# Kernel optimization log

Hardware: AMD Instinct MI355X
Metric: run time of the kernel (lower is better)

The kernel has to match this reference:

```python
import jax, jax.numpy as jnp
import numpy as np

N, E, IN_DIM, HID, HEADS = 50000, 800000, 128, 16, 8
EPS_BN = 1e-5


def _gat_conv(x, edge_index, W, att_src, att_dst, bias, heads, out_ch, concat):
    # x: [N, F_in]; W: [heads*out_ch, F_in]; att_*: [heads, out_ch]
    n = x.shape[0]
    h = (x @ W.T).reshape(n, heads, out_ch)            # [N, H, C]
    a_src = (h * att_src[None]).sum(-1)                # [N, H]
    a_dst = (h * att_dst[None]).sum(-1)                # [N, H]
    src, dst = edge_index[0], edge_index[1]
    alpha = jax.nn.leaky_relu(a_src[src] + a_dst[dst], negative_slope=0.2)  # [E, H]
    # segment softmax over destination node (per head)
    amax = jax.ops.segment_max(alpha, dst, num_segments=n)
    amax = jnp.where(jnp.isfinite(amax), amax, 0.0)
    ex = jnp.exp(alpha - amax[dst])
    denom = jax.ops.segment_sum(ex, dst, num_segments=n)
    attn = ex / (denom[dst] + 1e-16)                   # [E, H]
    msg = h[src] * attn[:, :, None]                    # [E, H, C]
    out = jax.ops.segment_sum(msg, dst, num_segments=n)  # [N, H, C]
    out = out.reshape(n, heads * out_ch) if concat else out.mean(axis=1)
    return out + bias


def _bn_eval(h, mean, var, gamma, beta):
    return (h - mean) * jax.lax.rsqrt(var + EPS_BN) * gamma + beta


def setup_inputs() -> dict:
    key = jax.random.key(0)
    ks = jax.random.split(key, 16)
    s = 0.1
    inp = {
        "x": jax.random.normal(ks[0], (N, IN_DIM), jnp.float32),
        "edge_index": jax.random.randint(ks[1], (2, E), 0, N, jnp.int32),
        # layer 0: GATConv(128 -> 16, heads=8, concat)
        "w0": jax.random.normal(ks[2], (HEADS * HID, IN_DIM), jnp.float32) * s,
        "asrc0": jax.random.normal(ks[3], (HEADS, HID), jnp.float32) * s,
        "adst0": jax.random.normal(ks[4], (HEADS, HID), jnp.float32) * s,
        "b0": jnp.zeros((HEADS * HID,), jnp.float32),
        "skip0": jax.random.normal(ks[5], (HEADS * HID, IN_DIM), jnp.float32) * s,
        "bn0_g": jnp.ones((HEADS * HID,), jnp.float32),
        "bn0_b": jnp.zeros((HEADS * HID,), jnp.float32),
        "bn0_m": jax.random.normal(ks[6], (HEADS * HID,), jnp.float32) * s,
        "bn0_v": jax.random.uniform(ks[7], (HEADS * HID,), jnp.float32, 0.5, 1.5),
        # layer 1: GATConv(128 -> 16, heads=1, concat=False)
        "w1": jax.random.normal(ks[8], (HID, HEADS * HID), jnp.float32) * s,
        "asrc1": jax.random.normal(ks[9], (1, HID), jnp.float32) * s,
        "adst1": jax.random.normal(ks[10], (1, HID), jnp.float32) * s,
        "b1": jnp.zeros((HID,), jnp.float32),
        "skip1": jax.random.normal(ks[11], (HID, HEADS * HID), jnp.float32) * s,
        "bn1_g": jnp.ones((HID,), jnp.float32),
        "bn1_b": jnp.zeros((HID,), jnp.float32),
        "bn1_m": jax.random.normal(ks[12], (HID,), jnp.float32) * s,
        "bn1_v": jax.random.uniform(ks[13], (HID,), jnp.float32, 0.5, 1.5),
    }
    return inp


def reference(x, edge_index, w0, asrc0, adst0, b0, skip0, bn0_g, bn0_b, bn0_m, bn0_v,
              w1, asrc1, adst1, b1, skip1, bn1_g, bn1_b, bn1_m, bn1_v):
    # eval mode: dropout = identity, BN uses running stats
    h_in = x
    h = _gat_conv(h_in, edge_index, w0, asrc0, adst0, b0, HEADS, HID, True)   # [N, 128]
    h = _bn_eval(h, bn0_m, bn0_v, bn0_g, bn0_b)
    h = h + h_in @ skip0.T
    h = jax.nn.elu(h)
    h_in = h
    h = _gat_conv(h_in, edge_index, w1, asrc1, adst1, b1, 1, HID, False)      # [N, 16]
    h = _bn_eval(h, bn1_m, bn1_v, bn1_g, bn1_b)
    h = h + h_in @ skip1.T
    h = jax.nn.elu(h)
    return h
```

## Files before the change

### kernel.cpp

```cpp
#include <hip/hip_runtime.h>
#include <hip/hip_bf16.h>

#define NN 50000
#define EE 800000
#define INDIM 128
#define HIDC 16
#define NHEAD 8
#define COARSE 196
#define EPB 2048
#define CAPR 6144
#define CAPB 8192

typedef __attribute__((ext_vector_type(8))) short bf16x8;
typedef __attribute__((ext_vector_type(4))) float f32x4;

__device__ __forceinline__ float bf2f(unsigned short u) {
    union { float f; unsigned int i; } v; v.i = ((unsigned int)u) << 16; return v.f;
}
__device__ __forceinline__ unsigned short f2bf(float f) {
    union { float f; unsigned int i; } v; v.f = f;
    unsigned int r = v.i + 0x7FFFu + ((v.i >> 16) & 1u);
    return (unsigned short)(r >> 16);
}
__device__ __forceinline__ unsigned char f2fp8(float f) {
    return (unsigned char)(__builtin_amdgcn_cvt_pk_fp8_f32(f, f, 0, 0) & 0xFF);
}

__global__ __launch_bounds__(256) void k_cvt(const float* __restrict__ x,
                                             const float* __restrict__ w0,
                                             const float* __restrict__ skip0,
                                             const float* __restrict__ w1,
                                             const float* __restrict__ skip1,
                                             unsigned int* __restrict__ xb2,
                                             unsigned int* __restrict__ wb2,
                                             unsigned int* __restrict__ wb1_2,
                                             int* __restrict__ ccur)
{
    if (blockIdx.x == 0 && threadIdx.x < COARSE)
        ccur[threadIdx.x] = threadIdx.x * CAPR;

    const long NX = (long)NN * 128 / 4;
    const long NW = 256 * 128 / 4;
    const long NW1 = 32 * 128 / 4;
    long i = (long)blockIdx.x * 256 + threadIdx.x;
    if (i < NX) {
        float4 v = ((const float4*)x)[i];
        xb2[i * 2]     = (unsigned int)f2bf(v.x) | ((unsigned int)f2bf(v.y) << 16);
        xb2[i * 2 + 1] = (unsigned int)f2bf(v.z) | ((unsigned int)f2bf(v.w) << 16);
    } else if (i < NX + NW) {
        long j = i - NX;
        const float4* src = (j < 128 * 128 / 4) ? ((const float4*)w0 + j)
                                                : ((const float4*)skip0 + (j - 128 * 128 / 4));
        float4 v = *src;
        wb2[j * 2]     = (unsigned int)f2bf(v.x) | ((unsigned int)f2bf(v.y) << 16);
        wb2[j * 2 + 1] = (unsigned int)f2bf(v.z) | ((unsigned int)f2bf(v.w) << 16);
    } else if (i < NX + NW + NW1) {
        long j = i - NX - NW;
        const float4* src = (j < 16 * 128 / 4) ? ((const float4*)w1 + j)
                                               : ((const float4*)skip1 + (j - 16 * 128 / 4));
        float4 v = *src;
        wb1_2[j * 2]     = (unsigned int)f2bf(v.x) | ((unsigned int)f2bf(v.y) << 16);
        wb1_2[j * 2 + 1] = (unsigned int)f2bf(v.z) | ((unsigned int)f2bf(v.w) << 16);
    }
}

__global__ __launch_bounds__(256) void k_partA(const int* __restrict__ ei,
                                               int* __restrict__ ccur,
                                               unsigned int* __restrict__ pairs)
{
    __shared__ int bcnt[256];
    __shared__ int lofs[256];
    __shared__ int gofs[256];
    __shared__ unsigned int stage[EPB];
    __shared__ int gpos[EPB];
    const int t = threadIdx.x;
    const int e0 = blockIdx.x * EPB;

    bcnt[t] = 0;
    __syncthreads();

    int mybin[8], myrank[8];
    unsigned int mypair[8];
    #pragma unroll
    for (int k = 0; k < 8; k++) {
        int e = e0 + k * 256 + t;
        mybin[k] = -1;
        if (e < EE) {
            int s = ei[e], d = ei[EE + e];
            int b = d >> 8;
            myrank[k] = atomicAdd(&bcnt[b], 1);
            mybin[k] = b;
            mypair[k] = ((unsigned)d << 16) | (unsigned)s;
        }
    }
    __syncthreads();

    int v = bcnt[t];
    lofs[t] = v;
    __syncthreads();
    for (int off = 1; off < 256; off <<= 1) {
        int u = (t >= off) ? lofs[t - off] : 0;
        __syncthreads();
        lofs[t] += u;
        __syncthreads();
    }
    if (t < COARSE && v > 0) gofs[t] = atomicAdd(&ccur[t], v);
    __syncthreads();

    #pragma unroll
    for (int k = 0; k < 8; k++) {
        int b = mybin[k];
        if (b >= 0) {
            int slot = (lofs[b] - bcnt[b]) + myrank[k];
            stage[slot] = mypair[k];
            gpos[slot]  = gofs[b] + myrank[k];
        }
    }
    __syncthreads();

    const int total = lofs[255];
    for (int i = t; i < total; i += 256)
        pairs[gpos[i]] = stage[i];
}

__global__ __launch_bounds__(256) void k_partB(const unsigned int* __restrict__ pairs,
                                               const int* __restrict__ ccur,
                                               unsigned short* __restrict__ srcidx,
                                               int* __restrict__ rowbeg,
                                               int* __restrict__ deg)
{
    __shared__ int fcnt[256], fofs[256], fcur[256];
    __shared__ unsigned short stage[CAPB];
    const int b = blockIdx.x, t = threadIdx.x;
    const int beg = b * CAPR;
    int cnt = ccur[b] - beg;
    if (cnt > CAPR) cnt = CAPR;

    fcnt[t] = 0;
    __syncthreads();
    for (int i = t; i < cnt; i += 256) {
        unsigned int d = pairs[beg + i] >> 16;
        atomicAdd(&fcnt[d & 255], 1);
    }
    __syncthreads();

    int v = fcnt[t];
    fofs[t] = v;
    __syncthreads();
    for (int off = 1; off < 256; off <<= 1) {
        int u = (t >= off) ? fofs[t - off] : 0;
        __syncthreads();
        fofs[t] += u;
        __syncthreads();
    }
    int ex = fofs[t] - v;
    int node = b * 256 + t;
    if (node < NN) { rowbeg[node] = beg + ex; deg[node] = v; }
    fcur[t] = ex;
    __syncthreads();

    for (int i = t; i < cnt; i += 256) {
        unsigned int p = pairs[beg + i];
        unsigned int d = p >> 16;
        int slot = atomicAdd(&fcur[d & 255], 1);
        stage[slot] = (unsigned short)(p & 0xFFFFu);
    }
    __syncthreads();
    for (int i = t; i < cnt; i += 256)
        srcidx[beg + i] = stage[i];
}

__global__ __launch_bounds__(256) void k_gemm0(
    const unsigned short* __restrict__ xb, const unsigned short* __restrict__ wb,
    const float* __restrict__ asrc0, const float* __restrict__ adst0,
    unsigned char* __restrict__ h0f, unsigned short* __restrict__ s0b,
    float* __restrict__ a_src0, float* __restrict__ a_dst0)
{
    const int wave = threadIdx.x >> 6;
    const int lane = threadIdx.x & 63;
    const int lrow = lane & 15;
    const int quad = lane >> 4;
    const int rowbase = blockIdx.x * 64;

    bf16x8 bfrag[4][4];
    float asv[4], adv[4];
    #pragma unroll
    for (int t = 0; t < 4; t++) {
        const int jg = wave * 64 + t * 16 + lrow;
        #pragma unroll
        for (int ki = 0; ki < 4; ki++)
            bfrag[t][ki] = *(const bf16x8*)(wb + (long)jg * 128 + ki * 32 + quad * 8);
        if (wave < 2) { asv[t] = asrc0[jg]; adv[t] = adst0[jg]; }
    }

    #pragma unroll
    for (int sub = 0; sub < 4; sub++) {
        const int row0 = rowbase + sub * 16;
        if (row0 >= NN) break;
        const unsigned short* xrow = xb + (long)(row0 + lrow) * 128;
        bf16x8 afrag[4];
        #pragma unroll
        for (int ki = 0; ki < 4; ki++)
            afrag[ki] = *(const bf16x8*)(xrow + ki * 32 + quad * 8);

        f32x4 acc[4];
        #pragma unroll
        for (int t = 0; t < 4; t++) acc[t] = (f32x4){0.f, 0.f, 0.f, 0.f};

        #pragma unroll
        for (int ki = 0; ki < 4; ki++)
            #pragma unroll
            for (int t = 0; t < 4; t++)
                acc[t] = __builtin_amdgcn_mfma_f32_16x16x32_bf16(afrag[ki], bfrag[t][ki], acc[t], 0, 0, 0);

        if (wave < 2) {
            #pragma unroll
            for (int t = 0; t < 4; t++) {
                const int jg = wave * 64 + t * 16 + lrow;
                #pragma unroll
                for (int r = 0; r < 4; r++) {
                    const int n = row0 + quad * 4 + r;
                    float val = acc[t][r];
                    h0f[(long)n * 128 + jg] = f2fp8(val);
                    float ps = val * asv[t];
                    float pd = val * adv[t];
                    ps += __shfl_xor(ps, 1); ps += __shfl_xor(ps, 2);
                    ps += __shfl_xor(ps, 4); ps += __shfl_xor(ps, 8);
                    pd += __shfl_xor(pd, 1); pd += __shfl_xor(pd, 2);
                    pd += __shfl_xor(pd, 4); pd += __shfl_xor(pd, 8);
                    if (lrow == 0) {
                        const int h = wave * 4 + t;
                        a_src0[(long)n * 8 + h] = ps;
                        a_dst0[(long)n * 8 + h] = pd;
                    }
                }
            }
        } else {
            #pragma unroll
            for (int t = 0; t < 4; t++) {
                const int jg = wave * 64 + t * 16 + lrow - 128;
                #pragma unroll
                for (int r = 0; r < 4; r++) {
                    const int n = row0 + quad * 4 + r;
                    s0b[(long)n * 128 + jg] = f2bf(acc[t][r]);
                }
            }
        }
    }
}

__global__ __launch_bounds__(256) void k_agg0(
    const int* __restrict__ rowbeg, const int* __restrict__ deg,
    const unsigned short* __restrict__ srcidx,
    const unsigned char* __restrict__ h0f, const float* __restrict__ a_src0,
    const float* __restrict__ a_dst0, unsigned int* __restrict__ out0b2)
{
    const int d = (blockIdx.x * 256 + threadIdx.x) >> 6;
    if (d >= NN) return;
    const int lane = threadIdx.x & 63;
    const int beg = rowbeg[d], end = beg + deg[d];
    const int eslot = lane >> 3;
    const int hph1 = lane & 7;
    const int c = lane * 2;
    const int hsel = lane >> 3;
    const float adst = a_dst0[(long)d * 8 + hph1];

    float den = 0.f;
    float2 accA = {0.f, 0.f}, accB = {0.f, 0.f};
    for (int i = beg; i < end; i += 16) {
        const int idxA = i + eslot;
        const int idxB = i + 8 + eslot;
        const bool vA = idxA < end;
        const bool vB = idxB < end;
        const int sA = vA ? (int)srcidx[idxA] : 0;
        const int sB = vB ? (int)srcidx[idxB] : 0;
        float aA = a_src0[(long)sA * 8 + hph1] + adst;
        float aB = a_src0[(long)sB * 8 + hph1] + adst;
        aA = aA > 0.f ? aA : 0.2f * aA;
        aB = aB > 0.f ? aB : 0.2f * aB;
        const float wA = vA ? __expf(aA) : 0.f;
        const float wB = vB ? __expf(aB) : 0.f;
        den += wA + wB;
        #pragma unroll
        for (int j = 0; j < 8; j++) {
            const float wjA = __shfl(wA, j * 8 + hsel);
            const int sjA = __shfl(sA, j * 8);
            const float wjB = __shfl(wB, j * 8 + hsel);
            const int sjB = __shfl(sB, j * 8);
            const unsigned int uA = *(const unsigned short*)(h0f + (long)sjA * 128 + c);
            const unsigned int uB = *(const unsigned short*)(h0f + (long)sjB * 128 + c);
            accA.x += wjA * __builtin_amdgcn_cvt_f32_fp8(uA, 0);
            accA.y += wjA * __builtin_amdgcn_cvt_f32_fp8(uA, 1);
            accB.x += wjB * __builtin_amdgcn_cvt_f32_fp8(uB, 0);
            accB.y += wjB * __builtin_amdgcn_cvt_f32_fp8(uB, 1);
        }
    }
    float2 acc = {accA.x + accB.x, accA.y + accB.y};
    den += __shfl_xor(den, 8);
    den += __shfl_xor(den, 16);
    den += __shfl_xor(den, 32);
    const float denh = __shfl(den, hsel);
    const float inv = 1.f / (denh + 1e-16f);
    out0b2[(long)d * 64 + lane] =
        (unsigned int)f2bf(acc.x * inv) | ((unsigned int)f2bf(acc.y * inv) << 16);
}

__global__ __launch_bounds__(256) void k_post0(
    const unsigned short* __restrict__ out0b, const unsigned short* __restrict__ s0b,
    const float* __restrict__ b0, const float* __restrict__ g0,
    const float* __restrict__ bb0, const float* __restrict__ m0,
    const float* __restrict__ v0,
    const unsigned short* __restrict__ wb1,
    const float* __restrict__ asrc1, const float* __restrict__ adst1,
    unsigned short* __restrict__ h1b, float* __restrict__ s1,
    float* __restrict__ a_src1, float* __restrict__ a_dst1)
{
    __shared__ float Ac[128], Bc[128];
    const int tid = threadIdx.x;
    if (tid < 128) {
        float A = g0[tid] * rsqrtf(v0[tid] + 1e-5f);
        Ac[tid] = A;
        Bc[tid] = (b0[tid] - m0[tid]) * A + bb0[tid];
    }
    __syncthreads();

    const int lane = tid & 63, wave = tid >> 6;
    const int lrow = lane & 15, quad = lane >> 4;

    bf16x8 bfrag[2][4];
    #pragma unroll
    for (int t = 0; t < 2; t++)
        #pragma unroll
        for (int ki = 0; ki < 4; ki++)
            bfrag[t][ki] = *(const bf16x8*)(wb1 + (long)(t * 16 + lrow) * 128 + ki * 32 + quad * 8);
    const float avec = asrc1[lrow];
    const float dvec = adst1[lrow];

    const int tile = blockIdx.x * 4 + wave;
    if (tile * 16 >= NN) return;
    const int n0 = tile * 16;
    const long arow = (long)(n0 + lrow) * 128;

    bf16x8 afrag[4];
    #pragma unroll
    for (int ki = 0; ki < 4; ki++) {
        const int ch = ki * 32 + quad * 8;
        uint4 uo = *(const uint4*)(out0b + arow + ch);
        uint4 us = *(const uint4*)(s0b + arow + ch);
        const unsigned int uov[4] = {uo.x, uo.y, uo.z, uo.w};
        const unsigned int usv[4] = {us.x, us.y, us.z, us.w};
        bf16x8 af;
        #pragma unroll
        for (int e = 0; e < 4; e++) {
            const int c0 = ch + e * 2, c1 = c0 + 1;
            float x0 = bf2f((unsigned short)uov[e]) * Ac[c0] + Bc[c0] + bf2f((unsigned short)usv[e]);
            float x1 = bf2f((unsigned short)(uov[e] >> 16)) * Ac[c1] + Bc[c1] + bf2f((unsigned short)(usv[e] >> 16));
            x0 = x0 > 0.f ? x0 : __expf(x0) - 1.f;
            x1 = x1 > 0.f ? x1 : __expf(x1) - 1.f;
            af[e * 2]     = (short)f2bf(x0);
            af[e * 2 + 1] = (short)f2bf(x1);
        }
        afrag[ki] = af;
    }

    f32x4 acc0 = (f32x4){0.f, 0.f, 0.f, 0.f};
    f32x4 acc1 = (f32x4){0.f, 0.f, 0.f, 0.f};
    #pragma unroll
    for (int ki = 0; ki < 4; ki++) {
        acc0 = __builtin_amdgcn_mfma_f32_16x16x32_bf16(afrag[ki], bfrag[0][ki], acc0, 0, 0, 0);
        acc1 = __builtin_amdgcn_mfma_f32_16x16x32_bf16(afrag[ki], bfrag[1][ki], acc1, 0, 0, 0);
    }

    #pragma unroll
    for (int r = 0; r < 4; r++) {
        const int node = n0 + quad * 4 + r;
        h1b[(long)node * 16 + lrow] = f2bf(acc0[r]);
        s1[(long)node * 16 + lrow] = acc1[r];
        float ps = acc0[r] * avec;
        float pd = acc0[r] * dvec;
        ps += __shfl_xor(ps, 1); ps += __shfl_xor(ps, 2);
        ps += __shfl_xor(ps, 4); ps += __shfl_xor(ps, 8);
        pd += __shfl_xor(pd, 1); pd += __shfl_xor(pd, 2);
        pd += __shfl_xor(pd, 4); pd += __shfl_xor(pd, 8);
        if (lrow == 0) { a_src1[node] = ps; a_dst1[node] = pd; }
    }
}

__global__ __launch_bounds__(256) void k_agg1_final(
    const int* __restrict__ rowbeg, const int* __restrict__ deg,
    const unsigned short* __restrict__ srcidx,
    const unsigned short* __restrict__ h1b, const float* __restrict__ a_src1,
    const float* __restrict__ a_dst1, const float* __restrict__ s1,
    const float* __restrict__ b1, const float* __restrict__ g1,
    const float* __restrict__ bb1, const float* __restrict__ m1,
    const float* __restrict__ v1, float* __restrict__ out)
{
    const int gid = blockIdx.x * 256 + threadIdx.x;
    const int d = gid >> 3;
    if (d >= NN) return;
    const int lane = threadIdx.x & 63;
    const int gl = lane & 7;
    const int gb = lane & ~7;
    const int c0 = gl * 2, c1 = c0 + 1;
    const int beg = rowbeg[d], end = beg + deg[d];
    const float adst = a_dst1[d];

    float den = 0.f;
    float2 accA = {0.f, 0.f}, accB = {0.f, 0.f};
    for (int i = beg; i < end; i += 16) {
        const int idxA = i + gl;
        const int idxB = i + 8 + gl;
        const bool vA = idxA < end;
        const bool vB = idxB < end;
        const int sA = vA ? (int)srcidx[idxA] : 0;
        const int sB = vB ? (int)srcidx[idxB] : 0;
        float aA = a_src1[sA] + adst;
        float aB = a_src1[sB] + adst;
        aA = aA > 0.f ? aA : 0.2f * aA;
        aB = aB > 0.f ? aB : 0.2f * aB;
        const float wA = vA ? __expf(aA) : 0.f;
        const float wB = vB ? __expf(aB) : 0.f;
        den += wA + wB;
        #pragma unroll
        for (int j = 0; j < 8; j++) {
            const float wjA = __shfl(wA, gb | j);
            const int sjA = __shfl(sA, gb | j);
            const float wjB = __shfl(wB, gb | j);
            const int sjB = __shfl(sB, gb | j);
            const unsigned int uA = *(const unsigned int*)(h1b + (long)sjA * 16 + c0);
            const unsigned int uB = *(const unsigned int*)(h1b + (long)sjB * 16 + c0);
            accA.x += wjA * bf2f((unsigned short)uA);
            accA.y += wjA * bf2f((unsigned short)(uA >> 16));
            accB.x += wjB * bf2f((unsigned short)uB);
            accB.y += wjB * bf2f((unsigned short)(uB >> 16));
        }
    }
    float2 acc = {accA.x + accB.x, accA.y + accB.y};
    den += __shfl_xor(den, 1);
    den += __shfl_xor(den, 2);
    den += __shfl_xor(den, 4);
    const float inv = 1.f / (den + 1e-16f);

    const float A0 = g1[c0] * rsqrtf(v1[c0] + 1e-5f);
    const float B0 = (b1[c0] - m1[c0]) * A0 + bb1[c0];
    const float A1 = g1[c1] * rsqrtf(v1[c1] + 1e-5f);
    const float B1 = (b1[c1] - m1[c1]) * A1 + bb1[c1];
    float2 sv = *(const float2*)(s1 + (long)d * 16 + c0);
    float v0o = acc.x * inv * A0 + B0 + sv.x;
    float v1o = acc.y * inv * A1 + B1 + sv.y;
    v0o = v0o > 0.f ? v0o : __expf(v0o) - 1.f;
    v1o = v1o > 0.f ? v1o : __expf(v1o) - 1.f;
    *(float2*)(out + (long)d * 16 + c0) = make_float2(v0o, v1o);
}

extern "C" void kernel_launch(void* const* d_in, const int* in_sizes, int n_in,
                              void* d_out, int out_size, void* d_ws, size_t ws_size,
                              hipStream_t stream)
{
    (void)in_sizes; (void)n_in; (void)out_size; (void)ws_size;
    const float* x     = (const float*)d_in[0];
    const int*   ei    = (const int*)d_in[1];
    const float* w0    = (const float*)d_in[2];
    const float* asrc0 = (const float*)d_in[3];
    const float* adst0 = (const float*)d_in[4];
    const float* b0    = (const float*)d_in[5];
    const float* skip0 = (const float*)d_in[6];
    const float* bn0g  = (const float*)d_in[7];
    const float* bn0b  = (const float*)d_in[8];
    const float* bn0m  = (const float*)d_in[9];
    const float* bn0v  = (const float*)d_in[10];
    const float* w1    = (const float*)d_in[11];
    const float* asrc1 = (const float*)d_in[12];
    const float* adst1 = (const float*)d_in[13];
    const float* b1    = (const float*)d_in[14];
    const float* skip1 = (const float*)d_in[15];
    const float* bn1g  = (const float*)d_in[16];
    const float* bn1b  = (const float*)d_in[17];
    const float* bn1m  = (const float*)d_in[18];
    const float* bn1v  = (const float*)d_in[19];

    const long NPAIR = (long)COARSE * CAPR;
    unsigned int* pairs = (unsigned int*)d_ws;
    unsigned short* xb    = (unsigned short*)(pairs + NPAIR);
    unsigned short* wb    = xb + (long)NN * 128;
    unsigned short* wb1   = wb + 256 * 128;
    unsigned short* s0b   = wb1 + 32 * 128;
    unsigned short* out0b = s0b + (long)NN * 128;
    unsigned short* h1b   = out0b + (long)NN * 128;
    unsigned short* srcidx= h1b + (long)NN * 16;
    unsigned char*  h0f   = (unsigned char*)(srcidx + NPAIR);
    float* a_src0 = (float*)(h0f + (long)NN * 128);
    float* a_dst0 = a_src0 + (long)NN * 8;
    float* s1     = a_dst0 + (long)NN * 8;
    float* a_src1 = s1 + (long)NN * 16;
    float* a_dst1 = a_src1 + NN;
    int* ccur   = (int*)(a_dst1 + NN);
    int* rowbeg = ccur + COARSE;
    int* deg    = rowbeg + NN;

    const long NTOT = (long)NN * 128 / 4 + 256 * 128 / 4 + 32 * 128 / 4;
    k_cvt<<<(unsigned)((NTOT + 255) / 256), 256, 0, stream>>>(
        x, w0, skip0, w1, skip1,
        (unsigned int*)xb, (unsigned int*)wb, (unsigned int*)wb1, ccur);

    k_partA<<<(EE + EPB - 1) / EPB, 256, 0, stream>>>(ei, ccur, pairs);
    k_partB<<<COARSE, 256, 0, stream>>>(pairs, ccur, srcidx, rowbeg, deg);

    k_gemm0<<<(NN + 63) / 64, 256, 0, stream>>>(xb, wb, asrc0, adst0,
                                                h0f, s0b, a_src0, a_dst0);
    k_agg0<<<(NN * 64 + 255) / 256, 256, 0, stream>>>(rowbeg, deg, srcidx, h0f,
                                                      a_src0, a_dst0, (unsigned int*)out0b);
    k_post0<<<(NN / 16 + 3) / 4, 256, 0, stream>>>(out0b, s0b, b0, bn0g, bn0b, bn0m, bn0v,
                                                   wb1, asrc1, adst1, h1b, s1, a_src1, a_dst1);
    k_agg1_final<<<(NN * 8 + 255) / 256, 256, 0, stream>>>(rowbeg, deg, srcidx, h1b,
                                                           a_src1, a_dst1, s1,
                                                           b1, bn1g, bn1b, bn1m, bn1v,
                                                           (float*)d_out);
}
```

Measured before the change: 218.2 us.

## Transpose MFMA operands in gemm0 for packed row-contiguous stores

Swaps the A and B operands of the MFMA in the first-layer GEMM so that each lane holds four consecutive output columns of a single node. The FP8 h0 values and BF16 skip values can then be written as packed 4-byte and 8-byte stores instead of scattered single-element stores, and the attention dot products are reduced with two cross-quad shuffles instead of four. It also halves rows per block (64 to 32) to launch twice as many blocks. The change targets store efficiency in the GEMM epilogue; the smaller tile reloads the weight fragments more often per row.

```diff
diff --git a/kernel.cpp b/kernel.cpp
--- a/kernel.cpp
+++ b/kernel.cpp
@@ -21,9 +21,6 @@
     union { float f; unsigned int i; } v; v.f = f;
     unsigned int r = v.i + 0x7FFFu + ((v.i >> 16) & 1u);
     return (unsigned short)(r >> 16);
-}
-__device__ __forceinline__ unsigned char f2fp8(float f) {
-    return (unsigned char)(__builtin_amdgcn_cvt_pk_fp8_f32(f, f, 0, 0) & 0xFF);
 }
 
 __global__ __launch_bounds__(256) void k_cvt(const float* __restrict__ x,
@@ -180,21 +177,25 @@
     const int lane = threadIdx.x & 63;
     const int lrow = lane & 15;
     const int quad = lane >> 4;
-    const int rowbase = blockIdx.x * 64;
+    const int rowbase = blockIdx.x * 32;
 
     bf16x8 bfrag[4][4];
-    float asv[4], adv[4];
+    float4 asv[4], adv[4];
     #pragma unroll
     for (int t = 0; t < 4; t++) {
         const int jg = wave * 64 + t * 16 + lrow;
         #pragma unroll
         for (int ki = 0; ki < 4; ki++)
             bfrag[t][ki] = *(const bf16x8*)(wb + (long)jg * 128 + ki * 32 + quad * 8);
-        if (wave < 2) { asv[t] = asrc0[jg]; adv[t] = adst0[jg]; }
-    }
-
-    #pragma unroll
-    for (int sub = 0; sub < 4; sub++) {
+        if (wave < 2) {
+            const int cb = wave * 64 + t * 16 + quad * 4;
+            asv[t] = *(const float4*)(asrc0 + cb);
+            adv[t] = *(const float4*)(adst0 + cb);
+        }
+    }
+
+    #pragma unroll
+    for (int sub = 0; sub < 2; sub++) {
         const int row0 = rowbase + sub * 16;
         if (row0 >= NN) break;
         const unsigned short* xrow = xb + (long)(row0 + lrow) * 128;
@@ -211,39 +212,36 @@
         for (int ki = 0; ki < 4; ki++)
             #pragma unroll
             for (int t = 0; t < 4; t++)
-                acc[t] = __builtin_amdgcn_mfma_f32_16x16x32_bf16(afrag[ki], bfrag[t][ki], acc[t], 0, 0, 0);
-
+                acc[t] = __builtin_amdgcn_mfma_f32_16x16x32_bf16(bfrag[t][ki], afrag[ki], acc[t], 0, 0, 0);
+
+        const int node = row0 + lrow;
         if (wave < 2) {
             #pragma unroll
             for (int t = 0; t < 4; t++) {
-                const int jg = wave * 64 + t * 16 + lrow;
-                #pragma unroll
-                for (int r = 0; r < 4; r++) {
-                    const int n = row0 + quad * 4 + r;
-                    float val = acc[t][r];
-                    h0f[(long)n * 128 + jg] = f2fp8(val);
-                    float ps = val * asv[t];
-                    float pd = val * adv[t];
-                    ps += __shfl_xor(ps, 1); ps += __shfl_xor(ps, 2);
-                    ps += __shfl_xor(ps, 4); ps += __shfl_xor(ps, 8);
-                    pd += __shfl_xor(pd, 1); pd += __shfl_xor(pd, 2);
-                    pd += __shfl_xor(pd, 4); pd += __shfl_xor(pd, 8);
-                    if (lrow == 0) {
-                        const int h = wave * 4 + t;
-                        a_src0[(long)n * 8 + h] = ps;
-                        a_dst0[(long)n * 8 + h] = pd;
-                    }
+                const int cb = wave * 64 + t * 16 + quad * 4;
+                unsigned int u = __builtin_amdgcn_cvt_pk_fp8_f32(acc[t][0], acc[t][1], 0u, 0);
+                u = __builtin_amdgcn_cvt_pk_fp8_f32(acc[t][2], acc[t][3], u, 1);
+                *(unsigned int*)(h0f + (long)node * 128 + cb) = u;
+                float ps = acc[t][0] * asv[t].x + acc[t][1] * asv[t].y
+                         + acc[t][2] * asv[t].z + acc[t][3] * asv[t].w;
+                float pd = acc[t][0] * adv[t].x + acc[t][1] * adv[t].y
+                         + acc[t][2] * adv[t].z + acc[t][3] * adv[t].w;
+                ps += __shfl_xor(ps, 16); ps += __shfl_xor(ps, 32);
+                pd += __shfl_xor(pd, 16); pd += __shfl_xor(pd, 32);
+                if (quad == 0) {
+                    const int h = wave * 4 + t;
+                    a_src0[(long)node * 8 + h] = ps;
+                    a_dst0[(long)node * 8 + h] = pd;
                 }
             }
         } else {
             #pragma unroll
             for (int t = 0; t < 4; t++) {
-                const int jg = wave * 64 + t * 16 + lrow - 128;
-                #pragma unroll
-                for (int r = 0; r < 4; r++) {
-                    const int n = row0 + quad * 4 + r;
-                    s0b[(long)n * 128 + jg] = f2bf(acc[t][r]);
-                }
+                const int cb = (wave - 2) * 64 + t * 16 + quad * 4;
+                uint2 u;
+                u.x = (unsigned int)f2bf(acc[t][0]) | ((unsigned int)f2bf(acc[t][1]) << 16);
+                u.y = (unsigned int)f2bf(acc[t][2]) | ((unsigned int)f2bf(acc[t][3]) << 16);
+                *(uint2*)(s0b + (long)node * 128 + cb) = u;
             }
         }
     }
@@ -506,7 +504,7 @@
     k_partA<<<(EE + EPB - 1) / EPB, 256, 0, stream>>>(ei, ccur, pairs);
     k_partB<<<COARSE, 256, 0, stream>>>(pairs, ccur, srcidx, rowbeg, deg);
 
-    k_gemm0<<<(NN + 63) / 64, 256, 0, stream>>>(xb, wb, asrc0, adst0,
+    k_gemm0<<<(NN + 31) / 32, 256, 0, stream>>>(xb, wb, asrc0, adst0,
                                                 h0f, s0b, a_src0, a_dst0);
     k_agg0<<<(NN * 64 + 255) / 256, 256, 0, stream>>>(rowbeg, deg, srcidx, h0f,
                                                       a_src0, a_dst0, (unsigned int*)out0b);
```

New measurement: 218.5 us. No clear change (+0.1%).
